# Kernel optimization log

Hardware: AMD Instinct MI355X
Metric: run time of the kernel (lower is better)

## Reference

```python
import jax, jax.numpy as jnp
import numpy as np

N_HEADS = 8
D_K = 64
SCALE = D_K ** -0.5


def setup_inputs() -> dict:
    key = jax.random.key(0)
    ks = jax.random.split(key, 5)
    B, C, H, W = 4, 512, 32, 32
    x = jax.random.normal(ks[0], (B, C, H, W), dtype=jnp.float32)
    Wp = jax.random.normal(ks[1], (3 * N_HEADS * D_K, C), dtype=jnp.float32) * (C ** -0.5)
    bp = jax.random.normal(ks[2], (3 * N_HEADS * D_K,), dtype=jnp.float32) * 0.02
    Wo = jax.random.normal(ks[3], (C, N_HEADS * D_K), dtype=jnp.float32) * ((N_HEADS * D_K) ** -0.5)
    bo = jax.random.normal(ks[4], (C,), dtype=jnp.float32) * 0.02
    return {"x": x, "Wp": Wp, "bp": bp, "Wo": Wo, "bo": bo}


def reference(x, Wp, bp, Wo, bo):
    # x: [B, C, H, W]; NOTE: the torch module defines GroupNorm but never calls it.
    B, C, H, W = x.shape
    s = H * W
    xs = x.reshape(B, C, s).transpose(0, 2, 1)          # [B, s, C]
    qkv = (xs @ Wp.T + bp).reshape(B, s, N_HEADS, 3 * D_K)
    q, k, v = jnp.split(qkv, 3, axis=-1)                 # each [B, s, h, d]
    attn = jnp.einsum('bihd,bjhd->bijh', q, k) * SCALE   # [B, s, s, h]
    attn = jax.nn.softmax(attn, axis=2)                  # softmax over j (keys)
    res = jnp.einsum('bijh,bjhd->bihd', attn, v)         # [B, s, h, d]
    res = res.reshape(B, s, N_HEADS * D_K)
    out = res @ Wo.T + bo + xs                           # residual add
    return out.transpose(0, 2, 1).reshape(B, C, H, W)
```

## Files before the change

kernel.cpp:

```cpp
#include <hip/hip_runtime.h>
#include <hip/hip_bf16.h>

typedef unsigned short u16;
typedef __attribute__((ext_vector_type(8))) short frag_ab;
typedef __attribute__((ext_vector_type(4))) float f32x4;
typedef _Float16 f16;
typedef __attribute__((ext_vector_type(4))) _Float16 f16x4;

#define LOG2E 1.44269504088896f

__device__ __forceinline__ float fast_exp2(float x) {
    return __builtin_amdgcn_exp2f(x);
}

__device__ __forceinline__ void gload_lds16(const u16* g, u16* s) {
    __builtin_amdgcn_global_load_lds((const __attribute__((address_space(1))) void*)g,
                                     (__attribute__((address_space(3))) void*)s, 16, 0, 0);
}
__device__ __forceinline__ void gload_lds16h(const f16* g, f16* s) {
    __builtin_amdgcn_global_load_lds((const __attribute__((address_space(1))) void*)g,
                                     (__attribute__((address_space(3))) void*)s, 16, 0, 0);
}

__device__ __forceinline__ void gemm128_bt_mainloop(
    const u16* __restrict__ A, const u16* __restrict__ B, int K,
    int m0, int n0, f32x4 acc[4][4], u16* As, u16* Bs)
{
    const int tid = threadIdx.x;
    const int lane = tid & 63, quad = lane >> 4, l16 = lane & 15;
    const int wr = ((tid >> 7) & 1) * 64;
    const int wc = ((tid >> 6) & 1) * 64;
    const int srow = tid >> 3;
    const int scol = (tid & 7) * 8;

    for (int k0 = 0; k0 < K; k0 += 64) {
        __syncthreads();
        #pragma unroll
        for (int p = 0; p < 4; ++p) {
            const int r = srow + p * 32;
            gload_lds16(A + (size_t)(m0 + r) * K + k0 + scol, As + r * 64 + scol);
        }
        #pragma unroll
        for (int p = 0; p < 4; ++p) {
            const int r = srow + p * 32;
            gload_lds16(B + (size_t)(n0 + r) * K + k0 + scol, Bs + r * 64 + scol);
        }
        __syncthreads();
        #pragma unroll
        for (int ks = 0; ks < 2; ++ks) {
            frag_ab a[4], b[4];
            #pragma unroll
            for (int mt = 0; mt < 4; ++mt)
                a[mt] = *(const frag_ab*)(As + (wr + mt * 16 + l16) * 64 + ks * 32 + quad * 8);
            #pragma unroll
            for (int nt = 0; nt < 4; ++nt)
                b[nt] = *(const frag_ab*)(Bs + (wc + nt * 16 + l16) * 64 + ks * 32 + quad * 8);
            #pragma unroll
            for (int mt = 0; mt < 4; ++mt)
                #pragma unroll
                for (int nt = 0; nt < 4; ++nt)
                    acc[mt][nt] = __builtin_amdgcn_mfma_f32_16x16x32_bf16(a[mt], b[nt], acc[mt][nt], 0, 0, 0);
        }
    }
}

__device__ __forceinline__ void gemm64x128_bt_mainloop(
    const u16* __restrict__ A, const u16* __restrict__ B, int K,
    int m0, int n0, f32x4 acc[2][4], u16* As, u16* Bs)
{
    const int tid = threadIdx.x;
    const int lane = tid & 63, quad = lane >> 4, l16 = lane & 15;
    const int wr = ((tid >> 7) & 1) * 32;
    const int wc = ((tid >> 6) & 1) * 64;
    const int srow = tid >> 3;
    const int scol = (tid & 7) * 8;

    for (int k0 = 0; k0 < K; k0 += 64) {
        __syncthreads();
        #pragma unroll
        for (int p = 0; p < 2; ++p) {
            const int r = srow + p * 32;
            gload_lds16(A + (size_t)(m0 + r) * K + k0 + scol, As + r * 64 + scol);
        }
        #pragma unroll
        for (int p = 0; p < 4; ++p) {
            const int r = srow + p * 32;
            gload_lds16(B + (size_t)(n0 + r) * K + k0 + scol, Bs + r * 64 + scol);
        }
        __syncthreads();
        #pragma unroll
        for (int ks = 0; ks < 2; ++ks) {
            frag_ab a[2], b[4];
            #pragma unroll
            for (int mt = 0; mt < 2; ++mt)
                a[mt] = *(const frag_ab*)(As + (wr + mt * 16 + l16) * 64 + ks * 32 + quad * 8);
            #pragma unroll
            for (int nt = 0; nt < 4; ++nt)
                b[nt] = *(const frag_ab*)(Bs + (wc + nt * 16 + l16) * 64 + ks * 32 + quad * 8);
            #pragma unroll
            for (int mt = 0; mt < 2; ++mt)
                #pragma unroll
                for (int nt = 0; nt < 4; ++nt)
                    acc[mt][nt] = __builtin_amdgcn_mfma_f32_16x16x32_bf16(a[mt], b[nt], acc[mt][nt], 0, 0, 0);
        }
    }
}

__global__ __launch_bounds__(256) void prep_kernel(
    const float* __restrict__ x, __hip_bfloat16* __restrict__ xs_bf,
    const float* __restrict__ Wp, const float* __restrict__ Wo,
    __hip_bfloat16* __restrict__ w_bf)
{
    __shared__ float tile[32][33];
    const int tid = threadIdx.x;
    const int id = blockIdx.x;
    if (id < 2048) {
        const int i0 = (id & 31) * 32;
        const int c0 = ((id >> 5) & 15) * 32;
        const int b  = id >> 9;
        const int tx = tid & 31, ty = tid >> 5;
        const float* xp = x + ((size_t)b * 512 + c0) * 1024 + i0;
        #pragma unroll
        for (int r = ty; r < 32; r += 8)
            tile[r][tx] = xp[(size_t)r * 1024 + tx];
        __syncthreads();
        __hip_bfloat16* op = xs_bf + ((size_t)b * 1024 + i0) * 512 + c0;
        #pragma unroll
        for (int r = ty; r < 32; r += 8)
            op[(size_t)r * 512 + tx] = __float2bfloat16(tile[tx][r]);
    } else {
        const int t = (id - 2048) * 256 + tid;
        const int i4 = t * 4;
        const float* src = (i4 < 786432) ? (Wp + i4) : (Wo + (i4 - 786432));
        const float4 v = *(const float4*)src;
        ushort4 o;
        o.x = __bfloat16_as_ushort(__float2bfloat16(v.x));
        o.y = __bfloat16_as_ushort(__float2bfloat16(v.y));
        o.z = __bfloat16_as_ushort(__float2bfloat16(v.z));
        o.w = __bfloat16_as_ushort(__float2bfloat16(v.w));
        *(ushort4*)((u16*)w_bf + i4) = o;
    }
}

__global__ __launch_bounds__(256) void qkv_gemm_kernel(
    const u16* __restrict__ Wpb, const u16* __restrict__ xsb,
    const float* __restrict__ bp,
    u16* __restrict__ Qb, u16* __restrict__ Kb, f16* __restrict__ VtT)
{
    __shared__ u16 As[128 * 64];
    __shared__ u16 Bs[128 * 64];
    __shared__ u16 Tr[4][64][72];
    f32x4 acc[4][4];
    #pragma unroll
    for (int mt = 0; mt < 4; ++mt)
        #pragma unroll
        for (int nt = 0; nt < 4; ++nt)
            { acc[mt][nt][0]=0.f; acc[mt][nt][1]=0.f; acc[mt][nt][2]=0.f; acc[mt][nt][3]=0.f; }
    const int m0 = blockIdx.x * 128;
    const int n0 = blockIdx.y * 128;
    gemm128_bt_mainloop(Wpb, xsb, 512, m0, n0, acc, As, Bs);

    const int tid = threadIdx.x;
    const int w = tid >> 6, lane = tid & 63, quad = lane >> 4, l16 = lane & 15;
    const int wr = ((tid >> 7) & 1) * 64, wc = ((tid >> 6) & 1) * 64;
    const int chbase = m0 + wr;
    const int pixb   = n0 + wc;
    const int ch64 = chbase >> 6;
    const int h = ch64 / 3, part = ch64 - h * 3;
    const int b = pixb >> 10, ipb = pixb & 1023;
    const size_t bh = (size_t)(b * 8 + h);

    if (part < 2) {
        const float scale = (part == 0) ? (0.125f * LOG2E) : 1.0f;
        u16* T = &Tr[w][0][0];
        #pragma unroll
        for (int nt = 0; nt < 4; ++nt) {
            const int pt = nt * 16 + l16;
            #pragma unroll
            for (int mt = 0; mt < 4; ++mt) {
                ushort4 pk;
                const int cb = chbase + mt * 16 + quad * 4;
                pk.x = __bfloat16_as_ushort(__float2bfloat16((acc[mt][nt][0] + bp[cb + 0]) * scale));
                pk.y = __bfloat16_as_ushort(__float2bfloat16((acc[mt][nt][1] + bp[cb + 1]) * scale));
                pk.z = __bfloat16_as_ushort(__float2bfloat16((acc[mt][nt][2] + bp[cb + 2]) * scale));
                pk.w = __bfloat16_as_ushort(__float2bfloat16((acc[mt][nt][3] + bp[cb + 3]) * scale));
                *(ushort4*)&T[pt * 72 + mt * 16 + quad * 4] = pk;
            }
        }
        u16* dst = (part == 0 ? Qb : Kb);
        #pragma unroll
        for (int p = 0; p < 8; ++p) {
            const int pt = p * 8 + (lane >> 3);
            const int ch8 = (lane & 7) * 8;
            uint4 rv = *(uint4*)&T[pt * 72 + ch8];
            *(uint4*)(dst + ((bh * 1024 + ipb + pt) << 6) + ch8) = rv;
        }
    } else {
        f16* dst = VtT + bh * 65536;
        #pragma unroll
        for (int mt = 0; mt < 4; ++mt) {
            #pragma unroll
            for (int r = 0; r < 4; ++r) {
                const int d = mt * 16 + quad * 4 + r;
                const float bias = bp[chbase + d];
                #pragma unroll
                for (int nt = 0; nt < 4; ++nt) {
                    const int j = ipb + nt * 16 + l16;
                    dst[(size_t)(j >> 3) * 512 + d * 8 + (j & 7)] =
                        (f16)(acc[mt][nt][r] + bias);
                }
            }
        }
    }
}

__global__ __launch_bounds__(256) void attn_kernel(
    const u16* __restrict__ Qb, const u16* __restrict__ Kb,
    const f16* __restrict__ VtT, __hip_bfloat16* __restrict__ resb)
{
    __shared__ u16 Ks[128 * 64];
    __shared__ f16 Vs[1024 * 8];
    const int bh = blockIdx.x;
    const int it = blockIdx.y;
    const int tid = threadIdx.x;
    const int w = tid >> 6, lane = tid & 63, quad = lane >> 4, l16 = lane & 15;
    const int srow = tid >> 3, scol = (tid & 7) * 8;

    const u16* Qp = Qb + (size_t)bh * 65536;
    const u16* Kp = Kb + (size_t)bh * 65536;
    const f16* Vp = VtT + (size_t)bh * 65536;

    frag_ab bq[2];
    {
        const u16* qptr = Qp + (size_t)(it * 64 + w * 16 + l16) * 64 + quad * 8;
        bq[0] = *(const frag_ab*)(qptr);
        bq[1] = *(const frag_ab*)(qptr + 32);
    }

    f32x4 o[4];
    #pragma unroll
    for (int dt = 0; dt < 4; ++dt) { o[dt][0]=0.f; o[dt][1]=0.f; o[dt][2]=0.f; o[dt][3]=0.f; }
    float l_lane = 0.f;

    for (int jt = 0; jt < 8; ++jt) {
        __syncthreads();
        #pragma unroll
        for (int p = 0; p < 4; ++p) {
            const int r = srow + p * 32;
            gload_lds16(Kp + (size_t)(jt * 128 + r) * 64 + scol, Ks + r * 64 + scol);
        }
        #pragma unroll
        for (int p = 0; p < 4; ++p) {
            const int c = (w * 4 + p) * 64;
            gload_lds16h(Vp + (size_t)((jt * 16 + w * 4 + p) * 64 + lane) * 8,
                         Vs + (size_t)(c + lane) * 8);
        }
        __syncthreads();

        f32x4 st[8];
        #pragma unroll
        for (int mt = 0; mt < 8; ++mt) { st[mt][0]=0.f; st[mt][1]=0.f; st[mt][2]=0.f; st[mt][3]=0.f; }
        #pragma unroll
        for (int mt = 0; mt < 8; ++mt) {
            frag_ab a0 = *(const frag_ab*)(Ks + (mt * 16 + l16) * 64 + quad * 8);
            frag_ab a1 = *(const frag_ab*)(Ks + (mt * 16 + l16) * 64 + 32 + quad * 8);
            st[mt] = __builtin_amdgcn_mfma_f32_16x16x32_bf16(a0, bq[0], st[mt], 0, 0, 0);
            st[mt] = __builtin_amdgcn_mfma_f32_16x16x32_bf16(a1, bq[1], st[mt], 0, 0, 0);
        }
        f16x4 pb[8];
        #pragma unroll
        for (int mt = 0; mt < 8; ++mt) {
            const float e0 = fast_exp2(st[mt][0]);
            const float e1 = fast_exp2(st[mt][1]);
            const float e2 = fast_exp2(st[mt][2]);
            const float e3 = fast_exp2(st[mt][3]);
            l_lane += (e0 + e1) + (e2 + e3);
            pb[mt][0] = (f16)e0; pb[mt][1] = (f16)e1;
            pb[mt][2] = (f16)e2; pb[mt][3] = (f16)e3;
        }
        #pragma unroll
        for (int ks = 0; ks < 8; ++ks) {
            const f16* vrow = Vs + (size_t)((2 * ks + (quad >> 1)) * 64) * 8 + (quad & 1) * 4;
            #pragma unroll
            for (int dt = 0; dt < 4; ++dt) {
                const f16x4 va = *(const f16x4*)(vrow + (dt * 16 + l16) * 8);
                o[dt] = __builtin_amdgcn_mfma_f32_16x16x16f16(va, pb[ks], o[dt], 0, 0, 0);
            }
        }
    }
    l_lane += __shfl_xor(l_lane, 16);
    l_lane += __shfl_xor(l_lane, 32);
    const float linv = 1.f / l_lane;

    __syncthreads();
    u16* T = Ks + w * 16 * 72;
    #pragma unroll
    for (int dt = 0; dt < 4; ++dt)
        #pragma unroll
        for (int r = 0; r < 4; ++r)
            T[l16 * 72 + dt * 16 + quad * 4 + r] =
                __bfloat16_as_ushort(__float2bfloat16(o[dt][r] * linv));
    const int ri = lane >> 2, c0 = (lane & 3) * 16;
    uint4 v0 = *(uint4*)&T[ri * 72 + c0];
    uint4 v1 = *(uint4*)&T[ri * 72 + c0 + 8];
    const int bb = bh >> 3, hh = bh & 7;
    u16* orow = (u16*)resb + ((size_t)(bb * 1024 + it * 64 + w * 16 + ri)) * 512 + hh * 64 + c0;
    *(uint4*)(orow) = v0;
    *(uint4*)(orow + 8) = v1;
}

__global__ __launch_bounds__(256) void out_gemm_kernel(
    const u16* __restrict__ Wob, const u16* __restrict__ resb,
    const float* __restrict__ bo, const float* __restrict__ x,
    float* __restrict__ out)
{
    __shared__ u16 As[64 * 64];
    __shared__ u16 Bs[128 * 64];
    f32x4 acc[2][4];
    #pragma unroll
    for (int mt = 0; mt < 2; ++mt)
        #pragma unroll
        for (int nt = 0; nt < 4; ++nt)
            { acc[mt][nt][0]=0.f; acc[mt][nt][1]=0.f; acc[mt][nt][2]=0.f; acc[mt][nt][3]=0.f; }
    const int m0 = blockIdx.x * 64;
    const int n0 = blockIdx.y * 128;
    gemm64x128_bt_mainloop(Wob, resb, 512, m0, n0, acc, As, Bs);

    const int tid = threadIdx.x;
    const int lane = tid & 63, quad = lane >> 4, l16 = lane & 15;
    const int wr = ((tid >> 7) & 1) * 32, wc = ((tid >> 6) & 1) * 64;
    #pragma unroll
    for (int nt = 0; nt < 4; ++nt) {
        const int pix = n0 + wc + nt * 16 + l16;
        const int b = pix >> 10, ip = pix & 1023;
        #pragma unroll
        for (int mt = 0; mt < 2; ++mt) {
            #pragma unroll
            for (int r = 0; r < 4; ++r) {
                const int c = m0 + wr + mt * 16 + quad * 4 + r;
                const size_t oidx = (((size_t)b * 512 + c) << 10) + ip;
                out[oidx] = acc[mt][nt][r] + bo[c] + x[oidx];
            }
        }
    }
}

extern "C" void kernel_launch(void* const* d_in, const int* in_sizes, int n_in,
                              void* d_out, int out_size, void* d_ws, size_t ws_size,
                              hipStream_t stream)
{
    const float* x  = (const float*)d_in[0];
    const float* Wp = (const float*)d_in[1];
    const float* bp = (const float*)d_in[2];
    const float* Wo = (const float*)d_in[3];
    const float* bo = (const float*)d_in[4];
    float* out = (float*)d_out;

    char* ws = (char*)d_ws;
    size_t off = 0;
    auto carve = [&](size_t bytes) -> void* {
        void* ptr = ws + off;
        off += (bytes + 255) & ~(size_t)255;
        return ptr;
    };
    __hip_bfloat16* xs_bf = (__hip_bfloat16*)carve((size_t)4096 * 512 * 2);
    __hip_bfloat16* Wp_bf = (__hip_bfloat16*)carve((size_t)1536 * 512 * 2);
    __hip_bfloat16* Wo_bf = (__hip_bfloat16*)carve((size_t)512 * 512 * 2);
    u16*            Qb    = (u16*)carve((size_t)32 * 1024 * 64 * 2);
    u16*            Kb    = (u16*)carve((size_t)32 * 1024 * 64 * 2);
    f16*            VtT   = (f16*)carve((size_t)32 * 1024 * 64 * 2);
    __hip_bfloat16* resb  = (__hip_bfloat16*)carve((size_t)4096 * 512 * 2);

    prep_kernel<<<dim3(3072), 256, 0, stream>>>(x, xs_bf, Wp, Wo, Wp_bf);
    qkv_gemm_kernel<<<dim3(12, 32), 256, 0, stream>>>(
        (const u16*)Wp_bf, (const u16*)xs_bf, bp, Qb, Kb, VtT);
    attn_kernel<<<dim3(32, 16), 256, 0, stream>>>(Qb, Kb, VtT, resb);
    out_gemm_kernel<<<dim3(8, 32), 256, 0, stream>>>(
        (const u16*)Wo_bf, (const u16*)resb, bo, x, out);
    (void)Wo_bf; (void)ws_size; (void)in_sizes; (void)n_in; (void)out_size;
}
```

Before: 121.4 us.

## Split attention keys across waves and reduce partial outputs in LDS

Changes the attention kernel's work split. Each wave used to own 16 query rows and walk all 128 keys per tile. Now each wave owns 32 keys of each tile for all 64 queries, and the per-wave partial outputs and row sums are combined through shared memory at the end. This cuts LDS reads of K and V fragments per wave and drops the per-tile 8-way score buffer. In exchange it adds registers for 16 output accumulators, a sizeable LDS reduction buffer that may lower occupancy, and an extra reduction pass.

Result: faster. 116.9 us (-3.7%).

```diff
diff --git a/kernel.cpp b/kernel.cpp
--- a/kernel.cpp
+++ b/kernel.cpp
@@ -219,7 +219,9 @@
     const f16* __restrict__ VtT, __hip_bfloat16* __restrict__ resb)
 {
     __shared__ u16 Ks[128 * 64];
-    __shared__ f16 Vs[1024 * 8];
+    __shared__ f16 Vs[16 * 64 * 8];
+    __shared__ float Opart[4][32][68];
+    __shared__ float Lpart[4][4][16];
     const int bh = blockIdx.x;
     const int it = blockIdx.y;
     const int tid = threadIdx.x;
@@ -230,17 +232,21 @@
     const u16* Kp = Kb + (size_t)bh * 65536;
     const f16* Vp = VtT + (size_t)bh * 65536;
 
-    frag_ab bq[2];
-    {
-        const u16* qptr = Qp + (size_t)(it * 64 + w * 16 + l16) * 64 + quad * 8;
-        bq[0] = *(const frag_ab*)(qptr);
-        bq[1] = *(const frag_ab*)(qptr + 32);
-    }
-
-    f32x4 o[4];
-    #pragma unroll
-    for (int dt = 0; dt < 4; ++dt) { o[dt][0]=0.f; o[dt][1]=0.f; o[dt][2]=0.f; o[dt][3]=0.f; }
-    float l_lane = 0.f;
+    frag_ab bq[4][2];
+    #pragma unroll
+    for (int ig = 0; ig < 4; ++ig) {
+        const u16* qptr = Qp + (size_t)(it * 64 + ig * 16 + l16) * 64 + quad * 8;
+        bq[ig][0] = *(const frag_ab*)(qptr);
+        bq[ig][1] = *(const frag_ab*)(qptr + 32);
+    }
+
+    f32x4 o[4][4];
+    #pragma unroll
+    for (int ig = 0; ig < 4; ++ig)
+        #pragma unroll
+        for (int dt = 0; dt < 4; ++dt)
+            { o[ig][dt][0]=0.f; o[ig][dt][1]=0.f; o[ig][dt][2]=0.f; o[ig][dt][3]=0.f; }
+    float l_acc[4] = {0.f, 0.f, 0.f, 0.f};
 
     for (int jt = 0; jt < 8; ++jt) {
         __syncthreads();
@@ -251,62 +257,96 @@
         }
         #pragma unroll
         for (int p = 0; p < 4; ++p) {
-            const int c = (w * 4 + p) * 64;
-            gload_lds16h(Vp + (size_t)((jt * 16 + w * 4 + p) * 64 + lane) * 8,
-                         Vs + (size_t)(c + lane) * 8);
-        }
-        __syncthreads();
-
-        f32x4 st[8];
-        #pragma unroll
-        for (int mt = 0; mt < 8; ++mt) { st[mt][0]=0.f; st[mt][1]=0.f; st[mt][2]=0.f; st[mt][3]=0.f; }
-        #pragma unroll
-        for (int mt = 0; mt < 8; ++mt) {
-            frag_ab a0 = *(const frag_ab*)(Ks + (mt * 16 + l16) * 64 + quad * 8);
-            frag_ab a1 = *(const frag_ab*)(Ks + (mt * 16 + l16) * 64 + 32 + quad * 8);
-            st[mt] = __builtin_amdgcn_mfma_f32_16x16x32_bf16(a0, bq[0], st[mt], 0, 0, 0);
-            st[mt] = __builtin_amdgcn_mfma_f32_16x16x32_bf16(a1, bq[1], st[mt], 0, 0, 0);
-        }
-        f16x4 pb[8];
-        #pragma unroll
-        for (int mt = 0; mt < 8; ++mt) {
-            const float e0 = fast_exp2(st[mt][0]);
-            const float e1 = fast_exp2(st[mt][1]);
-            const float e2 = fast_exp2(st[mt][2]);
-            const float e3 = fast_exp2(st[mt][3]);
-            l_lane += (e0 + e1) + (e2 + e3);
-            pb[mt][0] = (f16)e0; pb[mt][1] = (f16)e1;
-            pb[mt][2] = (f16)e2; pb[mt][3] = (f16)e3;
-        }
-        #pragma unroll
-        for (int ks = 0; ks < 8; ++ks) {
-            const f16* vrow = Vs + (size_t)((2 * ks + (quad >> 1)) * 64) * 8 + (quad & 1) * 4;
+            const int c = w * 4 + p;
+            gload_lds16h(Vp + (size_t)((jt * 16 + c) * 64 + lane) * 8,
+                         Vs + (size_t)(c * 64 + lane) * 8);
+        }
+        __syncthreads();
+
+        frag_ab ka[2][2];
+        #pragma unroll
+        for (int mt = 0; mt < 2; ++mt) {
+            const u16* kp = Ks + (w * 32 + mt * 16 + l16) * 64 + quad * 8;
+            ka[mt][0] = *(const frag_ab*)(kp);
+            ka[mt][1] = *(const frag_ab*)(kp + 32);
+        }
+        f16x4 va[4][2];
+        #pragma unroll
+        for (int ks = 0; ks < 2; ++ks) {
+            const f16* vrow = Vs + (size_t)(w * 4 + ks * 2 + (quad >> 1)) * 512 + (quad & 1) * 4;
+            #pragma unroll
+            for (int dt = 0; dt < 4; ++dt)
+                va[dt][ks] = *(const f16x4*)(vrow + (dt * 16 + l16) * 8);
+        }
+        #pragma unroll
+        for (int ig = 0; ig < 4; ++ig) {
+            f32x4 st0 = {0.f, 0.f, 0.f, 0.f}, st1 = {0.f, 0.f, 0.f, 0.f};
+            st0 = __builtin_amdgcn_mfma_f32_16x16x32_bf16(ka[0][0], bq[ig][0], st0, 0, 0, 0);
+            st0 = __builtin_amdgcn_mfma_f32_16x16x32_bf16(ka[0][1], bq[ig][1], st0, 0, 0, 0);
+            st1 = __builtin_amdgcn_mfma_f32_16x16x32_bf16(ka[1][0], bq[ig][0], st1, 0, 0, 0);
+            st1 = __builtin_amdgcn_mfma_f32_16x16x32_bf16(ka[1][1], bq[ig][1], st1, 0, 0, 0);
+            f16x4 p0, p1;
+            float s = 0.f;
+            #pragma unroll
+            for (int r = 0; r < 4; ++r) {
+                const float e0 = fast_exp2(st0[r]);
+                const float e1 = fast_exp2(st1[r]);
+                s += e0 + e1;
+                p0[r] = (f16)e0;
+                p1[r] = (f16)e1;
+            }
+            l_acc[ig] += s;
             #pragma unroll
             for (int dt = 0; dt < 4; ++dt) {
-                const f16x4 va = *(const f16x4*)(vrow + (dt * 16 + l16) * 8);
-                o[dt] = __builtin_amdgcn_mfma_f32_16x16x16f16(va, pb[ks], o[dt], 0, 0, 0);
+                o[ig][dt] = __builtin_amdgcn_mfma_f32_16x16x16f16(va[dt][0], p0, o[ig][dt], 0, 0, 0);
+                o[ig][dt] = __builtin_amdgcn_mfma_f32_16x16x16f16(va[dt][1], p1, o[ig][dt], 0, 0, 0);
             }
         }
     }
-    l_lane += __shfl_xor(l_lane, 16);
-    l_lane += __shfl_xor(l_lane, 32);
-    const float linv = 1.f / l_lane;
-
-    __syncthreads();
-    u16* T = Ks + w * 16 * 72;
-    #pragma unroll
-    for (int dt = 0; dt < 4; ++dt)
-        #pragma unroll
-        for (int r = 0; r < 4; ++r)
-            T[l16 * 72 + dt * 16 + quad * 4 + r] =
-                __bfloat16_as_ushort(__float2bfloat16(o[dt][r] * linv));
-    const int ri = lane >> 2, c0 = (lane & 3) * 16;
-    uint4 v0 = *(uint4*)&T[ri * 72 + c0];
-    uint4 v1 = *(uint4*)&T[ri * 72 + c0 + 8];
+    #pragma unroll
+    for (int ig = 0; ig < 4; ++ig) {
+        l_acc[ig] += __shfl_xor(l_acc[ig], 16);
+        l_acc[ig] += __shfl_xor(l_acc[ig], 32);
+    }
+    if (lane < 16) {
+        #pragma unroll
+        for (int ig = 0; ig < 4; ++ig)
+            Lpart[w][ig][lane] = l_acc[ig];
+    }
+
     const int bb = bh >> 3, hh = bh & 7;
-    u16* orow = (u16*)resb + ((size_t)(bb * 1024 + it * 64 + w * 16 + ri)) * 512 + hh * 64 + c0;
-    *(uint4*)(orow) = v0;
-    *(uint4*)(orow + 8) = v1;
+    const int il = tid >> 3, d0 = (tid & 7) * 8;
+    #pragma unroll
+    for (int ph = 0; ph < 2; ++ph) {
+        __syncthreads();
+        #pragma unroll
+        for (int g = 0; g < 2; ++g) {
+            const int ig = ph * 2 + g;
+            #pragma unroll
+            for (int dt = 0; dt < 4; ++dt)
+                *(f32x4*)&Opart[w][g * 16 + l16][dt * 16 + quad * 4] = o[ig][dt];
+        }
+        __syncthreads();
+        f32x4 sa = *(const f32x4*)&Opart[0][il][d0];
+        f32x4 sb = *(const f32x4*)&Opart[0][il][d0 + 4];
+        #pragma unroll
+        for (int ww = 1; ww < 4; ++ww) {
+            sa += *(const f32x4*)&Opart[ww][il][d0];
+            sb += *(const f32x4*)&Opart[ww][il][d0 + 4];
+        }
+        const int ig = ph * 2 + (il >> 4);
+        const float linv = 1.f / (Lpart[0][ig][il & 15] + Lpart[1][ig][il & 15] +
+                                  Lpart[2][ig][il & 15] + Lpart[3][ig][il & 15]);
+        u16 pk[8];
+        #pragma unroll
+        for (int e = 0; e < 4; ++e) {
+            pk[e]     = __bfloat16_as_ushort(__float2bfloat16(sa[e] * linv));
+            pk[e + 4] = __bfloat16_as_ushort(__float2bfloat16(sb[e] * linv));
+        }
+        u16* orow = (u16*)resb +
+            ((size_t)(bb * 1024 + it * 64 + ph * 32 + il)) * 512 + hh * 64 + d0;
+        *(uint4*)orow = *(uint4*)pk;
+    }
 }
 
 __global__ __launch_bounds__(256) void out_gemm_kernel(
```
